# Kernel optimization log

Measured on AMD Instinct MI355X. Metric: run time of the kernel, lower is better.

## Reference

```python
import jax, jax.numpy as jnp
import numpy as np

BLOCKSIZE = 4096
OUT_FEATURES = 16384
IN_FEATURES = 4096
BATCH, SEQ = 4, 2048


def setup_inputs() -> dict:
    key = jax.random.key(0)
    k_x, k_w, k_a, k_b = jax.random.split(key, 4)
    x = jax.random.normal(k_x, (BATCH, SEQ, IN_FEATURES), dtype=jnp.float32)
    # quantized int8 weight stored as indices into the 256-entry codebook
    weight_q = jax.random.randint(k_w, (OUT_FEATURES, IN_FEATURES), 0, 256, dtype=jnp.int32)
    n_blocks = (OUT_FEATURES * IN_FEATURES) // BLOCKSIZE  # 16384
    absmax = jax.random.uniform(k_a, (n_blocks,), dtype=jnp.float32) + 0.5
    # bitsandbytes dynamic-map code: a sorted table of values in [-1, 1]
    code = jnp.linspace(-1.0, 1.0, 256, dtype=jnp.float32)
    bias = jax.random.normal(k_b, (OUT_FEATURES,), dtype=jnp.float32) * 0.02
    return {"x": x, "weight_q": weight_q, "absmax": absmax, "code": code, "bias": bias}


def dequantize_blockwise(weight_q, absmax, code):
    # codebook lookup then per-block absmax scaling
    flat = code[weight_q.reshape(-1)]                      # [out*in]
    flat = flat.reshape(-1, BLOCKSIZE) * absmax[:, None]   # [n_blocks, blocksize]
    return flat.reshape(weight_q.shape)                    # [out, in]


def reference(x, weight_q, absmax, code, bias):
    w = dequantize_blockwise(weight_q, absmax, code)       # [out, in] fp32
    # F.linear(x, w, bias) = x @ w.T + bias
    return jnp.einsum("bsi,oi->bso", x, w) + bias
```

## Files before the change

### kernel.cpp

```cpp
#include <hip/hip_runtime.h>
#include <hip/hip_bf16.h>
#include <stdint.h>

#define M_TOTAL 8192
#define N_TOTAL 16384
#define K_TOTAL 4096

#define BM 256
#define BN 256
#define BK 64
#define NKT (K_TOTAL / BK)

using f32x4  = __attribute__((ext_vector_type(4))) float;
using bf16x8 = __attribute__((ext_vector_type(8))) short;

#define UNROLL _Pragma("unroll")

__device__ __forceinline__ unsigned short f2bf(float f) {
    union { float f; unsigned u; } v; v.f = f;
    unsigned r = v.u + 0x7fffu + ((v.u >> 16) & 1u);
    return (unsigned short)(r >> 16);
}

__device__ __forceinline__ void gload_lds16(const void* g, void* l) {
    __builtin_amdgcn_global_load_lds(
        (const __attribute__((address_space(1))) unsigned int*)g,
        (__attribute__((address_space(3))) unsigned int*)l,
        16, 0, 0);
}

__global__ void dequant_w_kernel(const int* __restrict__ q,
                                 const float* __restrict__ am,
                                 const float* __restrict__ code,
                                 unsigned short* __restrict__ wb) {
    __shared__ float lc[256];
    if (threadIdx.x < 256) lc[threadIdx.x] = code[threadIdx.x];
    __syncthreads();
    const int total = (N_TOTAL / 4) * K_TOTAL;
    const int stride = gridDim.x * blockDim.x;
    for (int i = blockIdx.x * blockDim.x + threadIdx.x; i < total; i += stride) {
        int4 v = reinterpret_cast<const int4*>(q)[i];
        float a = am[i >> 10];
        ushort4 o;
        o.x = f2bf(lc[v.x & 255] * a);
        o.y = f2bf(lc[v.y & 255] * a);
        o.z = f2bf(lc[v.z & 255] * a);
        o.w = f2bf(lc[v.w & 255] * a);
        reinterpret_cast<ushort4*>(wb)[i] = o;
    }
}

__global__ void cvt_x_kernel(const float* __restrict__ x,
                             unsigned short* __restrict__ xb) {
    const int total = (M_TOTAL * K_TOTAL) / 4;
    const int stride = gridDim.x * blockDim.x;
    for (int i = blockIdx.x * blockDim.x + threadIdx.x; i < total; i += stride) {
        float4 v = reinterpret_cast<const float4*>(x)[i];
        ushort4 o;
        o.x = f2bf(v.x); o.y = f2bf(v.y); o.z = f2bf(v.z); o.w = f2bf(v.w);
        reinterpret_cast<ushort4*>(xb)[i] = o;
    }
}

#define LOAD_AH(DST, BUFI, MH)                                                    \
    UNROLL for (int mf = 0; mf < 4; ++mf)                                         \
        UNROLL for (int ks = 0; ks < 2; ++ks)                                     \
            DST[mf][ks] = *reinterpret_cast<const bf16x8*>(                       \
                &sA[BUFI][((MH)*128 + arow_base + mf*16)*BK +                     \
                          (((ks*4 + rslot_hi) ^ rslot_xor)*8)]);

#define LOAD_BH(DST, BUFI, NH)                                                    \
    UNROLL for (int nf = 0; nf < 2; ++nf)                                         \
        UNROLL for (int ks = 0; ks < 2; ++ks)                                     \
            DST[nf][ks] = *reinterpret_cast<const bf16x8*>(                       \
                &sB[BUFI][((NH)*128 + brow_base + nf*16)*BK +                     \
                          (((ks*4 + rslot_hi) ^ rslot_xor)*8)]);

#define MFMA_Q(MH, NH, AR, BR)                                                    \
    UNROLL for (int mf = 0; mf < 4; ++mf)                                         \
        UNROLL for (int nf = 0; nf < 2; ++nf) {                                   \
            acc[MH][mf][NH][nf] = __builtin_amdgcn_mfma_f32_16x16x32_bf16(        \
                AR[mf][0], BR[nf][0], acc[MH][mf][NH][nf], 0, 0, 0);              \
            acc[MH][mf][NH][nf] = __builtin_amdgcn_mfma_f32_16x16x32_bf16(        \
                AR[mf][1], BR[nf][1], acc[MH][mf][NH][nf], 0, 0, 0);              \
        }

__global__ __launch_bounds__(512, 2) void gemm_rp_kernel(
        const unsigned short* __restrict__ A,
        const unsigned short* __restrict__ B,
        const float* __restrict__ bias,
        float* __restrict__ C) {
    __shared__ __align__(16) unsigned short sA[2][BM * BK];
    __shared__ __align__(16) unsigned short sB[2][BN * BK];

    const int nwg = gridDim.x;
    const int bid = blockIdx.x;
    const int wg  = (bid & 7) * (nwg >> 3) + (bid >> 3);
    const int nbn = N_TOTAL / BN;
    const int brow = (wg / nbn) * BM;
    const int bcol = (wg % nbn) * BN;

    const int tid  = threadIdx.x;
    const int wid  = tid >> 6;
    const int lane = tid & 63;
    const int wm   = wid >> 2;
    const int wn   = wid & 3;

    const int srow = wid * 8 + (lane >> 3);
    const int scol = ((lane & 7) ^ (lane >> 3)) * 8;
    const unsigned short* Asrc = A + (long long)(brow + srow) * K_TOTAL + scol;
    const unsigned short* Bsrc = B + (long long)(bcol + srow) * K_TOTAL + scol;

    auto stA = [&](int h, int j, int kt, int b) {
        gload_lds16(Asrc + (long long)(h*128 + j*64) * K_TOTAL + kt*BK,
                    &sA[b][(h*128 + j*64)*BK + wid*512]);
    };
    auto stB = [&](int h, int j, int kt, int b) {
        gload_lds16(Bsrc + (long long)(h*128 + j*64) * K_TOTAL + kt*BK,
                    &sB[b][(h*128 + j*64)*BK + wid*512]);
    };
    auto stage_tile = [&](int kt, int b) {
        stA(0,0,kt,b); stA(0,1,kt,b); stA(1,0,kt,b); stA(1,1,kt,b);
        stB(0,0,kt,b); stB(0,1,kt,b); stB(1,0,kt,b); stB(1,1,kt,b);
    };

    const int arow_base = wm * 64 + (lane & 15);
    const int brow_base = wn * 32 + (lane & 15);
    const int rslot_hi  = lane >> 4;
    const int rslot_xor = lane & 7;

    f32x4 acc[2][4][2][2];
    UNROLL for (int mh = 0; mh < 2; ++mh)
        UNROLL for (int mf = 0; mf < 4; ++mf)
            UNROLL for (int nh = 0; nh < 2; ++nh)
                UNROLL for (int nf = 0; nf < 2; ++nf)
                    acc[mh][mf][nh][nf] = (f32x4){0.f, 0.f, 0.f, 0.f};

    bf16x8 a0_r[4][2], a1_r[4][2];
    bf16x8 b0_r[2][2], b1_r[2][2];

    stage_tile(0, 0);
    stage_tile(1, 1);
    asm volatile("s_waitcnt vmcnt(8)" ::: "memory");
    __builtin_amdgcn_s_barrier();
    LOAD_AH(a0_r, 0, 0);
    LOAD_BH(b0_r, 0, 0);

    for (int t = 0; t < NKT; ++t) {
        const int b = t & 1;

        LOAD_BH(b1_r, b, 1);
        LOAD_AH(a1_r, b, 1);

        __builtin_amdgcn_s_setprio(1);
        MFMA_Q(0, 0, a0_r, b0_r);
        MFMA_Q(0, 1, a0_r, b1_r);
        MFMA_Q(1, 1, a1_r, b1_r);
        __builtin_amdgcn_s_setprio(0);

        asm volatile("s_waitcnt lgkmcnt(0) vmcnt(0)" ::: "memory");
        __builtin_amdgcn_s_barrier();

        if (t + 2 < NKT) stage_tile(t + 2, b);

        LOAD_AH(a0_r, b ^ 1, 0);

        __builtin_amdgcn_s_setprio(1);
        MFMA_Q(1, 0, a1_r, b0_r);
        __builtin_amdgcn_s_setprio(0);

        LOAD_BH(b0_r, b ^ 1, 0);
    }

    const int crow0 = (lane >> 4) * 4;
    const int ccol  = lane & 15;
    UNROLL for (int mh = 0; mh < 2; ++mh)
        UNROLL for (int mf = 0; mf < 4; ++mf) {
            const long long row0 = (long long)brow + mh*128 + wm*64 + mf*16 + crow0;
            UNROLL for (int nh = 0; nh < 2; ++nh)
                UNROLL for (int nf = 0; nf < 2; ++nf) {
                    const int col = bcol + nh*128 + wn*32 + nf*16 + ccol;
                    const float bv = bias[col];
                    UNROLL for (int r = 0; r < 4; ++r)
                        C[(row0 + r) * N_TOTAL + col] = acc[mh][mf][nh][nf][r] + bv;
                }
        }
}

extern "C" void kernel_launch(void* const* d_in, const int* in_sizes, int n_in,
                              void* d_out, int out_size, void* d_ws, size_t ws_size,
                              hipStream_t stream) {
    const float* x      = (const float*)d_in[0];
    const int*   wq     = (const int*)  d_in[1];
    const float* absmax = (const float*)d_in[2];
    const float* code   = (const float*)d_in[3];
    const float* bias   = (const float*)d_in[4];
    float* out = (float*)d_out;

    unsigned short* wb = (unsigned short*)d_ws;
    unsigned short* xb = wb + (size_t)N_TOTAL * K_TOTAL;

    dequant_w_kernel<<<2048, 256, 0, stream>>>(wq, absmax, code, wb);
    cvt_x_kernel   <<<2048, 256, 0, stream>>>(x, xb);

    dim3 grid((M_TOTAL / BM) * (N_TOTAL / BN));
    gemm_rp_kernel<<<grid, 512, 0, stream>>>(xb, wb, bias, out);
}
```

Before: 1.278 ms.

## Split GEMM main loop into four barrier-gated phases interleaving staging with MFMA

Restructures the bf16 GEMM main loop into a two-tile unrolled body. Each tile is split into four phases separated by a barrier plus LDS wait. The global-to-LDS staging for the next tile is split into A and B halves and issued alongside the MFMA quadrants, instead of as one burst after a single barrier. The aim is to overlap global loads and LDS reads with matrix math more evenly. The cost is four barriers per tile instead of one, a possible LDS write/read race because the barrier precedes the per-wave lgkmcnt wait, and redundant clamped loads in the final iteration.

```diff
diff --git a/kernel.cpp b/kernel.cpp
--- a/kernel.cpp
+++ b/kernel.cpp
@@ -85,7 +85,36 @@
                 AR[mf][1], BR[nf][1], acc[MH][mf][NH][nf], 0, 0, 0);              \
         }
 
-__global__ __launch_bounds__(512, 2) void gemm_rp_kernel(
+#define GATE()                                                                    \
+    __builtin_amdgcn_s_barrier();                                                 \
+    asm volatile("s_waitcnt lgkmcnt(0)" ::: "memory");
+
+#define TILE_BODY(BUF, NBUF, BX, BY, TS)                                          \
+                                             \
+    GATE();                                                                       \
+    LOAD_BH(BY, BUF, 1);                                                          \
+    __builtin_amdgcn_s_setprio(1); MFMA_Q(0,0,a0_r,BX);                           \
+    __builtin_amdgcn_s_setprio(0);                                                \
+              \
+    GATE();                                                                       \
+    LOAD_AH(a1_r, BUF, 1);                                                        \
+    __builtin_amdgcn_s_setprio(1); MFMA_Q(0,1,a0_r,BY);                           \
+    __builtin_amdgcn_s_setprio(0);                                                \
+    asm volatile("s_waitcnt vmcnt(0)" ::: "memory");                              \
+               \
+    GATE();                                                                       \
+    LOAD_AH(a0_r, NBUF, 0);                                                       \
+    stA(0,0,TS,BUF); stA(0,1,TS,BUF); stA(1,0,TS,BUF); stA(1,1,TS,BUF);           \
+    __builtin_amdgcn_s_setprio(1); MFMA_Q(1,1,a1_r,BY);                           \
+    __builtin_amdgcn_s_setprio(0);                                                \
+            \
+    GATE();                                                                       \
+    LOAD_BH(BY, NBUF, 0);                                                         \
+    stB(0,0,TS,BUF); stB(0,1,TS,BUF); stB(1,0,TS,BUF); stB(1,1,TS,BUF);           \
+    __builtin_amdgcn_s_setprio(1); MFMA_Q(1,0,a1_r,BX);                           \
+    __builtin_amdgcn_s_setprio(0);
+
+__global__ __launch_bounds__(512, 2) void gemm_pl_kernel(
         const unsigned short* __restrict__ A,
         const unsigned short* __restrict__ B,
         const float* __restrict__ bias,
@@ -119,10 +148,6 @@
         gload_lds16(Bsrc + (long long)(h*128 + j*64) * K_TOTAL + kt*BK,
                     &sB[b][(h*128 + j*64)*BK + wid*512]);
     };
-    auto stage_tile = [&](int kt, int b) {
-        stA(0,0,kt,b); stA(0,1,kt,b); stA(1,0,kt,b); stA(1,1,kt,b);
-        stB(0,0,kt,b); stB(0,1,kt,b); stB(1,0,kt,b); stB(1,1,kt,b);
-    };
 
     const int arow_base = wm * 64 + (lane & 15);
     const int brow_base = wn * 32 + (lane & 15);
@@ -137,39 +162,23 @@
                     acc[mh][mf][nh][nf] = (f32x4){0.f, 0.f, 0.f, 0.f};
 
     bf16x8 a0_r[4][2], a1_r[4][2];
-    bf16x8 b0_r[2][2], b1_r[2][2];
-
-    stage_tile(0, 0);
-    stage_tile(1, 1);
+    bf16x8 bx_r[2][2], by_r[2][2];
+
+    stA(0,0,0,0); stA(0,1,0,0); stA(1,0,0,0); stA(1,1,0,0);
+    stB(0,0,0,0); stB(0,1,0,0); stB(1,0,0,0); stB(1,1,0,0);
+    stA(0,0,1,1); stA(0,1,1,1); stA(1,0,1,1); stA(1,1,1,1);
+    stB(0,0,1,1); stB(0,1,1,1); stB(1,0,1,1); stB(1,1,1,1);
     asm volatile("s_waitcnt vmcnt(8)" ::: "memory");
     __builtin_amdgcn_s_barrier();
     LOAD_AH(a0_r, 0, 0);
-    LOAD_BH(b0_r, 0, 0);
-
-    for (int t = 0; t < NKT; ++t) {
-        const int b = t & 1;
-
-        LOAD_BH(b1_r, b, 1);
-        LOAD_AH(a1_r, b, 1);
-
-        __builtin_amdgcn_s_setprio(1);
-        MFMA_Q(0, 0, a0_r, b0_r);
-        MFMA_Q(0, 1, a0_r, b1_r);
-        MFMA_Q(1, 1, a1_r, b1_r);
-        __builtin_amdgcn_s_setprio(0);
-
-        asm volatile("s_waitcnt lgkmcnt(0) vmcnt(0)" ::: "memory");
-        __builtin_amdgcn_s_barrier();
-
-        if (t + 2 < NKT) stage_tile(t + 2, b);
-
-        LOAD_AH(a0_r, b ^ 1, 0);
-
-        __builtin_amdgcn_s_setprio(1);
-        MFMA_Q(1, 0, a1_r, b0_r);
-        __builtin_amdgcn_s_setprio(0);
-
-        LOAD_BH(b0_r, b ^ 1, 0);
+    LOAD_BH(bx_r, 0, 0);
+
+    for (int it = 0; it < NKT/2; ++it) {
+        const int t0 = 2*it;
+        const int s0 = (t0+2 < NKT) ? t0+2 : NKT-1;
+        const int s1 = (t0+3 < NKT) ? t0+3 : NKT-1;
+        TILE_BODY(0, 1, bx_r, by_r, s0)
+        TILE_BODY(1, 0, by_r, bx_r, s1)
     }
 
     const int crow0 = (lane >> 4) * 4;
@@ -204,5 +213,5 @@
     cvt_x_kernel   <<<2048, 256, 0, stream>>>(x, xb);
 
     dim3 grid((M_TOTAL / BM) * (N_TOTAL / BN));
-    gemm_rp_kernel<<<grid, 512, 0, stream>>>(xb, wb, bias, out);
-}
+    gemm_pl_kernel<<<grid, 512, 0, stream>>>(xb, wb, bias, out);
+}
```

Measured after the change: 1.301 ms. No clear change (+1.8%).

## Switch GEMM to four-stage LDS pipeline with BK=32 and k-slot layout

Applied to the files above, without the earlier changes.

Halves the K tile to 32 and keeps four LDS buffers so three tiles are in flight, with one barrier per iteration instead of the split two-phase schedule. The LDS layout changes to k-slot-major planes, where each 8-element k chunk is stored contiguously across rows, and the XOR swizzle is dropped. The goal is to hide global latency more deeply and simplify the schedule. The cost is twice as many iterations and barriers, less MFMA work per barrier, and possible LDS bank conflicts on the new layout.

```diff
diff --git a/kernel.cpp b/kernel.cpp
--- a/kernel.cpp
+++ b/kernel.cpp
@@ -8,7 +8,7 @@
 
 #define BM 256
 #define BN 256
-#define BK 64
+#define BK 32
 #define NKT (K_TOTAL / BK)
 
 using f32x4  = __attribute__((ext_vector_type(4))) float;
@@ -62,36 +62,19 @@
     }
 }
 
-#define LOAD_AH(DST, BUFI, MH)                                                    \
-    UNROLL for (int mf = 0; mf < 4; ++mf)                                         \
-        UNROLL for (int ks = 0; ks < 2; ++ks)                                     \
-            DST[mf][ks] = *reinterpret_cast<const bf16x8*>(                       \
-                &sA[BUFI][((MH)*128 + arow_base + mf*16)*BK +                     \
-                          (((ks*4 + rslot_hi) ^ rslot_xor)*8)]);
 
-#define LOAD_BH(DST, BUFI, NH)                                                    \
-    UNROLL for (int nf = 0; nf < 2; ++nf)                                         \
-        UNROLL for (int ks = 0; ks < 2; ++ks)                                     \
-            DST[nf][ks] = *reinterpret_cast<const bf16x8*>(                       \
-                &sB[BUFI][((NH)*128 + brow_base + nf*16)*BK +                     \
-                          (((ks*4 + rslot_hi) ^ rslot_xor)*8)]);
+#define BOUNDARY(VMN)                                                             \
+    asm volatile("s_waitcnt vmcnt(" #VMN ")" ::: "memory");                       \
+    __builtin_amdgcn_s_barrier();                                                 \
+    asm volatile("" ::: "memory");
 
-#define MFMA_Q(MH, NH, AR, BR)                                                    \
-    UNROLL for (int mf = 0; mf < 4; ++mf)                                         \
-        UNROLL for (int nf = 0; nf < 2; ++nf) {                                   \
-            acc[MH][mf][NH][nf] = __builtin_amdgcn_mfma_f32_16x16x32_bf16(        \
-                AR[mf][0], BR[nf][0], acc[MH][mf][NH][nf], 0, 0, 0);              \
-            acc[MH][mf][NH][nf] = __builtin_amdgcn_mfma_f32_16x16x32_bf16(        \
-                AR[mf][1], BR[nf][1], acc[MH][mf][NH][nf], 0, 0, 0);              \
-        }
-
-__global__ __launch_bounds__(512, 2) void gemm_rp_kernel(
+__global__ __launch_bounds__(512, 2) void gemm4b_kernel(
         const unsigned short* __restrict__ A,
         const unsigned short* __restrict__ B,
         const float* __restrict__ bias,
         float* __restrict__ C) {
-    __shared__ __align__(16) unsigned short sA[2][BM * BK];
-    __shared__ __align__(16) unsigned short sB[2][BN * BK];
+    __shared__ __align__(16) unsigned short sA[4][BM * BK];
+    __shared__ __align__(16) unsigned short sB[4][BN * BK];
 
     const int nwg = gridDim.x;
     const int bid = blockIdx.x;
@@ -106,28 +89,26 @@
     const int wm   = wid >> 2;
     const int wn   = wid & 3;
 
-    const int srow = wid * 8 + (lane >> 3);
-    const int scol = ((lane & 7) ^ (lane >> 3)) * 8;
-    const unsigned short* Asrc = A + (long long)(brow + srow) * K_TOTAL + scol;
-    const unsigned short* Bsrc = B + (long long)(bcol + srow) * K_TOTAL + scol;
+    const unsigned short* pAl = A + (long long)(brow + lane) * K_TOTAL;
+    const unsigned short* pBl = B + (long long)(bcol + lane) * K_TOTAL;
 
-    auto stA = [&](int h, int j, int kt, int b) {
-        gload_lds16(Asrc + (long long)(h*128 + j*64) * K_TOTAL + kt*BK,
-                    &sA[b][(h*128 + j*64)*BK + wid*512]);
-    };
-    auto stB = [&](int h, int j, int kt, int b) {
-        gload_lds16(Bsrc + (long long)(h*128 + j*64) * K_TOTAL + kt*BK,
-                    &sB[b][(h*128 + j*64)*BK + wid*512]);
-    };
-    auto stage_tile = [&](int kt, int b) {
-        stA(0,0,kt,b); stA(0,1,kt,b); stA(1,0,kt,b); stA(1,1,kt,b);
-        stB(0,0,kt,b); stB(0,1,kt,b); stB(1,0,kt,b); stB(1,1,kt,b);
+    const int idx0 = wid * 2,     j0 = idx0 >> 2, s0 = idx0 & 3;
+    const int idx1 = wid * 2 + 1, j1 = idx1 >> 2, s1 = idx1 & 3;
+
+    auto stage = [&](int kt) {
+        const int sb = kt & 3;
+        gload_lds16(pAl + (long long)(j0 * 64) * K_TOTAL + kt * BK + s0 * 8,
+                    &sA[sb][s0 * 2048 + j0 * 512]);
+        gload_lds16(pAl + (long long)(j1 * 64) * K_TOTAL + kt * BK + s1 * 8,
+                    &sA[sb][s1 * 2048 + j1 * 512]);
+        gload_lds16(pBl + (long long)(j0 * 64) * K_TOTAL + kt * BK + s0 * 8,
+                    &sB[sb][s0 * 2048 + j0 * 512]);
+        gload_lds16(pBl + (long long)(j1 * 64) * K_TOTAL + kt * BK + s1 * 8,
+                    &sB[sb][s1 * 2048 + j1 * 512]);
     };
 
-    const int arow_base = wm * 64 + (lane & 15);
-    const int brow_base = wn * 32 + (lane & 15);
-    const int rslot_hi  = lane >> 4;
-    const int rslot_xor = lane & 7;
+    const int rsl = (lane >> 4) * 2048;
+    const int l15 = lane & 15;
 
     f32x4 acc[2][4][2][2];
     UNROLL for (int mh = 0; mh < 2; ++mh)
@@ -136,41 +117,38 @@
                 UNROLL for (int nf = 0; nf < 2; ++nf)
                     acc[mh][mf][nh][nf] = (f32x4){0.f, 0.f, 0.f, 0.f};
 
-    bf16x8 a0_r[4][2], a1_r[4][2];
-    bf16x8 b0_r[2][2], b1_r[2][2];
+    auto compute = [&](int t) {
+        const int rb = t & 3;
+        bf16x8 a_r[2][4], b_r[2][2];
+        UNROLL for (int mh = 0; mh < 2; ++mh)
+            UNROLL for (int mf = 0; mf < 4; ++mf)
+                a_r[mh][mf] = *reinterpret_cast<const bf16x8*>(
+                    &sA[rb][rsl + (mh*128 + wm*64 + mf*16 + l15) * 8]);
+        UNROLL for (int nh = 0; nh < 2; ++nh)
+            UNROLL for (int nf = 0; nf < 2; ++nf)
+                b_r[nh][nf] = *reinterpret_cast<const bf16x8*>(
+                    &sB[rb][rsl + (nh*128 + wn*32 + nf*16 + l15) * 8]);
+        __builtin_amdgcn_s_setprio(1);
+        UNROLL for (int mh = 0; mh < 2; ++mh)
+            UNROLL for (int mf = 0; mf < 4; ++mf)
+                UNROLL for (int nh = 0; nh < 2; ++nh)
+                    UNROLL for (int nf = 0; nf < 2; ++nf)
+                        acc[mh][mf][nh][nf] = __builtin_amdgcn_mfma_f32_16x16x32_bf16(
+                            a_r[mh][mf], b_r[nh][nf], acc[mh][mf][nh][nf], 0, 0, 0);
+        __builtin_amdgcn_s_setprio(0);
+    };
 
-    stage_tile(0, 0);
-    stage_tile(1, 1);
-    asm volatile("s_waitcnt vmcnt(8)" ::: "memory");
-    __builtin_amdgcn_s_barrier();
-    LOAD_AH(a0_r, 0, 0);
-    LOAD_BH(b0_r, 0, 0);
+    stage(0); stage(1); stage(2);
+    BOUNDARY(8)
 
-    for (int t = 0; t < NKT; ++t) {
-        const int b = t & 1;
-
-        LOAD_BH(b1_r, b, 1);
-        LOAD_AH(a1_r, b, 1);
-
-        __builtin_amdgcn_s_setprio(1);
-        MFMA_Q(0, 0, a0_r, b0_r);
-        MFMA_Q(0, 1, a0_r, b1_r);
-        MFMA_Q(1, 1, a1_r, b1_r);
-        __builtin_amdgcn_s_setprio(0);
-
-        asm volatile("s_waitcnt lgkmcnt(0) vmcnt(0)" ::: "memory");
-        __builtin_amdgcn_s_barrier();
-
-        if (t + 2 < NKT) stage_tile(t + 2, b);
-
-        LOAD_AH(a0_r, b ^ 1, 0);
-
-        __builtin_amdgcn_s_setprio(1);
-        MFMA_Q(1, 0, a1_r, b0_r);
-        __builtin_amdgcn_s_setprio(0);
-
-        LOAD_BH(b0_r, b ^ 1, 0);
+    for (int t = 0; t + 3 < NKT; ++t) {
+        stage(t + 3);
+        compute(t);
+        BOUNDARY(8)
     }
+    compute(NKT - 3); BOUNDARY(4)
+    compute(NKT - 2); BOUNDARY(0)
+    compute(NKT - 1);
 
     const int crow0 = (lane >> 4) * 4;
     const int ccol  = lane & 15;
@@ -204,5 +182,5 @@
     cvt_x_kernel   <<<2048, 256, 0, stream>>>(x, xb);
 
     dim3 grid((M_TOTAL / BM) * (N_TOTAL / BN));
-    gemm_rp_kernel<<<grid, 512, 0, stream>>>(xb, wb, bias, out);
+    gemm4b_kernel<<<grid, 512, 0, stream>>>(xb, wb, bias, out);
 }
```

Result: slower. 1.960 ms (+53.4%).
